# Performance work log

Hardware: AMD Instinct MI355X
Metric: run time of the kernel (lower is better)

The kernel has to match this reference:

```python
import jax, jax.numpy as jnp
import numpy as np

A = 40001         # atoms (+1 zero-padding row 0)
NB = 6            # max neighbors per atom (a2b width)
BN = 160001       # bonds (+1 zero-padding row 0)
ATOM_FDIM = 133
BOND_FDIM = 147
H = 300           # hidden_size (dim_embedding)
N_MOLS = 1000
A_SIZE = 40       # uniform atoms per molecule (a_scope)


def setup_inputs() -> dict:
    key = jax.random.key(0)
    ks = jax.random.split(key, 24)

    def w(k, shape, fan):
        return jax.random.normal(k, shape, dtype=jnp.float32) / np.sqrt(fan).astype(np.float32)

    f_atoms = jax.random.normal(ks[0], (A, ATOM_FDIM), dtype=jnp.float32).at[0].set(0.0)
    f_bonds = jax.random.normal(ks[1], (BN, BOND_FDIM), dtype=jnp.float32).at[0].set(0.0)
    a2b = jax.random.randint(ks[2], (A, NB), 0, BN, dtype=jnp.int32)
    b2a = jax.random.randint(ks[3], (BN,), 1, A, dtype=jnp.int32)
    b2revb = jax.random.randint(ks[4], (BN,), 1, BN, dtype=jnp.int32)

    return dict(
        f_atoms=f_atoms, f_bonds=f_bonds,
        Wi_atom=w(ks[5], (ATOM_FDIM, H), ATOM_FDIM),
        Wi_bond=w(ks[6], (BOND_FDIM, H), BOND_FDIM),
        Wh0=w(ks[7], (H, H), H),
        Wh1=w(ks[8], (H, H), H),
        W_lr=w(ks[9], (3 * H, H), 3 * H),
        W_o=w(ks[10], (2 * H, H), 2 * H),
        b_o=w(ks[11], (H,), H),
        gru_bias=w(ks[12], (H,), H),
        gWih_f=w(ks[13], (3 * H, H), H), gWhh_f=w(ks[14], (3 * H, H), H),
        gbih_f=w(ks[15], (3 * H,), H), gbhh_f=w(ks[16], (3 * H,), H),
        gWih_b=w(ks[17], (3 * H, H), H), gWhh_b=w(ks[18], (3 * H, H), H),
        gbih_b=w(ks[19], (3 * H,), H), gbhh_b=w(ks[20], (3 * H,), H),
        a2b=a2b, b2a=b2a, b2revb=b2revb,
        n_mols=N_MOLS, a_size=A_SIZE,
    )


def _gru_dir(x, h0, Wih, Whh, bih, bhh):
    """One direction of a torch-style GRU. x: [B,T,H], h0: [B,H] -> [B,T,H]."""
    xp = jnp.einsum('bth,gh->btg', x, Wih) + bih  # [B,T,3H], input proj precomputed

    def step(h, xt):
        gh = h @ Whh.T + bhh
        i_r, i_z, i_n = jnp.split(xt, 3, axis=-1)
        h_r, h_z, h_n = jnp.split(gh, 3, axis=-1)
        r = jax.nn.sigmoid(i_r + h_r)
        z = jax.nn.sigmoid(i_z + h_z)
        n = jnp.tanh(i_n + r * h_n)
        hn = (1.0 - z) * n + z * h
        return hn, hn

    _, ys = jax.lax.scan(step, h0, jnp.swapaxes(xp, 0, 1))
    return jnp.swapaxes(ys, 0, 1)


def _forward(f_atoms, f_bonds, Wi_atom, Wi_bond, Wh0, Wh1, W_lr, W_o, b_o, gru_bias,
             gWih_f, gWhh_f, gbih_f, gbhh_f, gWih_b, gWhh_b, gbih_b, gbhh_b,
             a2b, b2a, b2revb, n_mols, a_size):
    relu = jax.nn.relu
    input_atom = relu(f_atoms @ Wi_atom)              # [A,H]
    message_atom = input_atom
    input_bond = relu(f_bonds @ Wi_bond)              # [BN,H]
    message_bond = input_bond

    # depth-1 = 2 message passing steps (depth=3)
    for Wh in (Wh0, Wh1):
        nei = message_bond[a2b]                        # [A,NB,H] gather (index_select_ND)
        agg = nei.sum(axis=1) * nei.max(axis=1)        # sum * max neighbor aggregation
        message_atom = message_atom + agg
        mb = message_atom[b2a] - message_bond[b2revb]  # subtract reverse message
        message_bond = relu(input_bond + mb @ Wh)      # dropout p=0 -> identity

    nei = message_bond[a2b]
    agg = nei.sum(axis=1) * nei.max(axis=1)
    agg = jnp.concatenate([agg, message_atom, input_atom], axis=1) @ W_lr  # [A,H]

    # --- BatchGRU (uniform a_scope: mol i -> atoms [1+i*a_size, 1+(i+1)*a_size)) ---
    message = relu(agg + gru_bias)
    seqs = message[1:].reshape(n_mols, a_size, -1)     # padded per-mol sequences
    h0 = agg[1:].reshape(n_mols, a_size, -1).max(axis=1)  # init hidden = per-mol max
    out_f = _gru_dir(seqs, h0, gWih_f, gWhh_f, gbih_f, gbhh_f)
    out_b = _gru_dir(seqs[:, ::-1], h0, gWih_b, gWhh_b, gbih_b, gbhh_b)[:, ::-1]
    out = jnp.concatenate([out_f, out_b], axis=-1).reshape(n_mols * a_size, -1)  # [A-1,2H]
    pad0 = jnp.concatenate([message[0:1], message[0:1]], axis=1)  # padding row duplicated
    message2 = jnp.concatenate([pad0, out], axis=0)    # [A,2H]

    atom_hiddens = relu(message2 @ W_o + b_o)          # [A,H]
    mol_vecs = atom_hiddens[1:].reshape(n_mols, a_size, -1).mean(axis=1)  # [n_mols,H]
    return mol_vecs


def reference(f_atoms, f_bonds, Wi_atom, Wi_bond, Wh0, Wh1, W_lr, W_o, b_o, gru_bias,
              gWih_f, gWhh_f, gbih_f, gbhh_f, gWih_b, gWhh_b, gbih_b, gbhh_b,
              a2b, b2a, b2revb, n_mols, a_size):
    return _forward(f_atoms, f_bonds, Wi_atom, Wi_bond, Wh0, Wh1, W_lr, W_o, b_o, gru_bias,
                    gWih_f, gWhh_f, gbih_f, gbhh_f, gWih_b, gWhh_b, gbih_b, gbhh_b,
                    a2b, b2a, b2revb, n_mols, a_size)
```

## Files before the change

### kernel.cpp

```cpp
#include <hip/hip_runtime.h>
#include <math.h>

constexpr int A_TOT  = 40001;
constexpr int NB     = 6;
constexpr int BN_TOT = 160001;
constexpr int AF     = 133;
constexpr int BF     = 147;
constexpr int H      = 300;
constexpr int NMOL   = 1000;
constexpr int ASZ    = 40;

constexpr int PK_WH0 = 0;
constexpr int PK_WH1 = 90000;
constexpr int PK_WIB = 180000;
constexpr int PK_WIA = 224400;

template<int NR, int P>
__device__ __forceinline__ void gemv4(const float (*rows)[P], const float* __restrict__ W,
                                      int K, int f, float* __restrict__ acc)
{
    int k4 = 0;
    for (; k4 + 4 <= K; k4 += 4) {
        float w0 = W[(k4 + 0) * H + f];
        float w1 = W[(k4 + 1) * H + f];
        float w2 = W[(k4 + 2) * H + f];
        float w3 = W[(k4 + 3) * H + f];
#pragma unroll
        for (int i = 0; i < NR; ++i) {
            float4 b = *(const float4*)&rows[i][k4];
            acc[i] = fmaf(b.x, w0, fmaf(b.y, w1, fmaf(b.z, w2, fmaf(b.w, w3, acc[i]))));
        }
    }
    for (; k4 < K; ++k4) {
        float wv = W[k4 * H + f];
#pragma unroll
        for (int i = 0; i < NR; ++i) acc[i] = fmaf(rows[i][k4], wv, acc[i]);
    }
}

template<int NR, int P>
__device__ __forceinline__ void gemv4p(const float (*rows)[P], const float4* __restrict__ Pw,
                                       int K4, int f, float* __restrict__ acc)
{
#pragma clang loop unroll(disable)
    for (int k4i = 0; k4i < K4; ++k4i) {
        float4 w = Pw[k4i * 300 + f];
#pragma unroll
        for (int i = 0; i < NR; ++i) {
            float4 b = *(const float4*)&rows[i][k4i * 4];
            acc[i] = fmaf(b.x, w.x, fmaf(b.y, w.y, fmaf(b.z, w.z, fmaf(b.w, w.w, acc[i]))));
        }
    }
}

__global__ __launch_bounds__(256) void k_packmp(
    const float* __restrict__ s0, const float* __restrict__ s1,
    const float* __restrict__ s2, const float* __restrict__ s3,
    float* __restrict__ dout)
{
    const float* S[4] = {s0, s1, s2, s3};
    const int Ks[4]  = {300, 300, 147, 133};
    const int K4s[4] = {75, 75, 37, 34};
    const int off[4] = {PK_WH0, PK_WH1, PK_WIB, PK_WIA};
    int z = blockIdx.y;
    int o = blockIdx.x * 256 + threadIdx.x;
    int n = K4s[z] * 1200;
    if (o < n) {
        int k4 = o / 1200; int rem = o - k4 * 1200;
        int f = rem >> 2;  int j = rem & 3;
        int k = k4 * 4 + j;
        dout[off[z] + o] = (k < Ks[z]) ? S[z][(size_t)k * 300 + f] : 0.f;
    }
}

#define GA 4
__global__ __launch_bounds__(320) void k_msga1(
    const float* __restrict__ f_atoms, const float* __restrict__ f_bonds,
    const float4* __restrict__ PWia, const float4* __restrict__ PWib,
    const int* __restrict__ a2b, float* __restrict__ msgA1)
{
    __shared__ __align__(16) float fb[GA * NB][152];
    __shared__ __align__(16) float fa[GA][136];
    __shared__ int bidx[GA * NB];

    const int a0 = blockIdx.x * GA;
    const int tid = threadIdx.x;
    const int f = tid;

    if (tid < GA * NB) {
        int a = a0 + tid / NB;
        bidx[tid] = (a < A_TOT) ? a2b[a * NB + (tid % NB)] : 0;
    }
    __syncthreads();
    for (int idx = tid; idx < GA * NB * 148; idx += 320) {
        int i = idx / 148, k = idx - i * 148;
        fb[i][k] = (k < BF) ? f_bonds[(size_t)bidx[i] * BF + k] : 0.f;
    }
    for (int idx = tid; idx < GA * 136; idx += 320) {
        int l = idx / 136, k = idx - l * 136;
        int a = a0 + l;
        fa[l][k] = (a < A_TOT && k < AF) ? f_atoms[(size_t)a * AF + k] : 0.f;
    }
    __syncthreads();

    if (f < H) {
        float part[GA];
#pragma unroll
        for (int l = 0; l < GA; ++l) {
            float acc[NB];
#pragma unroll
            for (int j = 0; j < NB; ++j) acc[j] = 0.f;
            gemv4p<NB, 152>((const float (*)[152])&fb[l * NB], PWib, 37, f, acc);
            float s = 0.f, mx = -INFINITY;
#pragma unroll
            for (int j = 0; j < NB; ++j) {
                float x = fmaxf(acc[j], 0.f);
                s += x; mx = fmaxf(mx, x);
            }
            part[l] = s * mx;
        }
        float acc2[GA];
#pragma unroll
        for (int l = 0; l < GA; ++l) acc2[l] = 0.f;
        gemv4p<GA, 136>(fa, PWia, 34, f, acc2);
#pragma unroll
        for (int l = 0; l < GA; ++l) {
            int a = a0 + l;
            if (a < A_TOT) msgA1[(size_t)a * H + f] = fmaxf(acc2[l], 0.f) + part[l];
        }
    }
}

#define NR2 8
__global__ __launch_bounds__(320) void k_m1f(
    const float* __restrict__ f_bonds, const float4* __restrict__ PWib,
    const float4* __restrict__ PWh0, const float* __restrict__ msgA1,
    const int* __restrict__ b2a, const int* __restrict__ b2revb,
    float* __restrict__ m1)
{
    __shared__ __align__(16) float v[NR2][304];
    __shared__ __align__(16) float fbl[NR2][152];
    __shared__ int r_[NR2], q_[NR2], p_[NR2];

    const int r0 = blockIdx.x * NR2;
    const int tid = threadIdx.x;
    const int f = tid;

    if (tid < NR2) {
        int r = r0 + tid;
        if (r >= BN_TOT) r = 0;
        r_[tid] = r;
        q_[tid] = b2revb[r];
        p_[tid] = b2a[r];
    }
    __syncthreads();
    for (int idx = tid; idx < NR2 * 75; idx += 320) {
        int i = idx / 75, k4 = idx - i * 75;
        ((float4*)v[i])[k4] = ((const float4*)(msgA1 + (size_t)p_[i] * H))[k4];
    }
    for (int idx = tid; idx < NR2 * 148; idx += 320) {
        int i = idx / 148, k = idx - i * 148;
        fbl[i][k] = (k < BF) ? f_bonds[(size_t)q_[i] * BF + k] : 0.f;
    }
    __syncthreads();
    if (f < H) {
        float acc[NR2];
#pragma unroll
        for (int i = 0; i < NR2; ++i) acc[i] = 0.f;
        gemv4p<NR2, 152>(fbl, PWib, 37, f, acc);
#pragma unroll
        for (int i = 0; i < NR2; ++i) v[i][f] -= fmaxf(acc[i], 0.f);
    }
    __syncthreads();
    for (int idx = tid; idx < NR2 * 148; idx += 320) {
        int i = idx / 148, k = idx - i * 148;
        fbl[i][k] = (k < BF) ? f_bonds[(size_t)r_[i] * BF + k] : 0.f;
    }
    float accm[NR2];
#pragma unroll
    for (int i = 0; i < NR2; ++i) accm[i] = 0.f;
    if (f < H) gemv4p<NR2, 304>(v, PWh0, 75, f, accm);
    __syncthreads();
    if (f < H) {
        float accr[NR2];
#pragma unroll
        for (int i = 0; i < NR2; ++i) accr[i] = 0.f;
        gemv4p<NR2, 152>(fbl, PWib, 37, f, accr);
#pragma unroll
        for (int i = 0; i < NR2; ++i) {
            int r = r0 + i;
            if (r < BN_TOT)
                m1[(size_t)r * H + f] = fmaxf(fmaxf(accr[i], 0.f) + accm[i], 0.f);
        }
    }
}

__global__ __launch_bounds__(256) void k_msga2ef(
    const float* __restrict__ m1, const int* __restrict__ a2b, float* msgA)
{
    int idx = blockIdx.x * 256 + threadIdx.x;
    if (idx >= A_TOT * H) return;
    int a = idx / H;
    int f = idx - a * H;
    float s = 0.f, mx = -INFINITY;
#pragma unroll
    for (int j = 0; j < NB; ++j) {
        int r = a2b[a * NB + j];
        float v = m1[(size_t)r * H + f];
        s += v;
        mx = fmaxf(mx, v);
    }
    msgA[idx] += s * mx;
}

#define GC 2
#define RC (GC * NB)
__global__ __launch_bounds__(320) void k_aggl2f(
    const float* __restrict__ f_atoms, const float* __restrict__ f_bonds,
    const float4* __restrict__ PWia, const float4* __restrict__ PWib,
    const float4* __restrict__ PWh1, const float* __restrict__ W_lr,
    const float* __restrict__ msgA2, const float* __restrict__ m1,
    const int* __restrict__ a2b, const int* __restrict__ b2a,
    const int* __restrict__ b2revb, float* __restrict__ aggL)
{
    __shared__ __align__(16) float w[RC][304];
    __shared__ __align__(16) float fbl[RC][152];
    __shared__ __align__(16) float agg3r[GC][304];
    __shared__ __align__(16) float mA2r[GC][304];
    __shared__ __align__(16) float inAr[GC][304];
    __shared__ __align__(16) float fa[GC][136];
    __shared__ int b_[RC], rp_[RC], p2_[RC];

    const int a0 = blockIdx.x * GC;
    const int tid = threadIdx.x;
    const int f = tid;

    if (tid < RC) {
        int a = a0 + tid / NB;
        int b = (a < A_TOT) ? a2b[a * NB + (tid % NB)] : 0;
        b_[tid] = b;
        rp_[tid] = b2revb[b];
        p2_[tid] = b2a[b];
    }
    __syncthreads();
    for (int idx = tid; idx < RC * 75; idx += 320) {
        int i = idx / 75, k4 = idx - i * 75;
        float4 a4 = ((const float4*)(msgA2 + (size_t)p2_[i] * H))[k4];
        float4 b4 = ((const float4*)(m1 + (size_t)rp_[i] * H))[k4];
        ((float4*)w[i])[k4] = make_float4(a4.x - b4.x, a4.y - b4.y, a4.z - b4.z, a4.w - b4.w);
    }
    for (int idx = tid; idx < RC * 148; idx += 320) {
        int i = idx / 148, k = idx - i * 148;
        fbl[i][k] = (k < BF) ? f_bonds[(size_t)b_[i] * BF + k] : 0.f;
    }
    for (int idx = tid; idx < GC * 75; idx += 320) {
        int l = idx / 75, k4 = idx - l * 75;
        int a = a0 + l;
        ((float4*)mA2r[l])[k4] = (a < A_TOT) ? ((const float4*)(msgA2 + (size_t)a * H))[k4]
                                             : make_float4(0.f, 0.f, 0.f, 0.f);
    }
    for (int idx = tid; idx < GC * 136; idx += 320) {
        int l = idx / 136, k = idx - l * 136;
        int a = a0 + l;
        fa[l][k] = (a < A_TOT && k < AF) ? f_atoms[(size_t)a * AF + k] : 0.f;
    }
    __syncthreads();

    if (f < H) {
        float accm[RC];
#pragma unroll
        for (int i = 0; i < RC; ++i) accm[i] = 0.f;
        gemv4p<RC, 304>(w, PWh1, 75, f, accm);
        float accb[RC];
#pragma unroll
        for (int i = 0; i < RC; ++i) accb[i] = 0.f;
        gemv4p<RC, 152>(fbl, PWib, 37, f, accb);
#pragma unroll
        for (int l = 0; l < GC; ++l) {
            float s = 0.f, mx = -INFINITY;
#pragma unroll
            for (int j = 0; j < NB; ++j) {
                int i = l * NB + j;
                float m2 = fmaxf(fmaxf(accb[i], 0.f) + accm[i], 0.f);
                s += m2; mx = fmaxf(mx, m2);
            }
            agg3r[l][f] = s * mx;
        }
        float acc2[GC];
#pragma unroll
        for (int l = 0; l < GC; ++l) acc2[l] = 0.f;
        gemv4p<GC, 136>(fa, PWia, 34, f, acc2);
#pragma unroll
        for (int l = 0; l < GC; ++l) inAr[l][f] = fmaxf(acc2[l], 0.f);
    }
    __syncthreads();

    if (f < H) {
        float accL[GC];
#pragma unroll
        for (int l = 0; l < GC; ++l) accL[l] = 0.f;
        gemv4<GC, 304>(agg3r, W_lr,            H, f, accL);
        gemv4<GC, 304>(mA2r, W_lr + 300 * 300, H, f, accL);
        gemv4<GC, 304>(inAr, W_lr + 600 * 300, H, f, accL);
#pragma unroll
        for (int l = 0; l < GC; ++l) {
            int a = a0 + l;
            if (a < A_TOT) aggL[(size_t)a * H + f] = accL[l];
        }
    }
}

#define GB 4
#define RB (GB * NB)
__global__ __launch_bounds__(320) void k_msga2b(
    const float* __restrict__ f_bonds, const float* __restrict__ Wi_bond,
    const float* __restrict__ Wh0,
    const float* __restrict__ msgA1, float* __restrict__ msgA2,
    const int* __restrict__ a2b, const int* __restrict__ b2a,
    const int* __restrict__ b2revb)
{
    __shared__ __align__(16) float v[RB][304];
    __shared__ __align__(16) float fbl[RB][152];
    __shared__ int r_[RB], q_[RB], p_[RB];

    const int a0 = blockIdx.x * GB;
    const int tid = threadIdx.x;
    const int f = tid;

    if (tid < RB) {
        int a = a0 + tid / NB;
        int r = (a < A_TOT) ? a2b[a * NB + (tid % NB)] : 0;
        r_[tid] = r;
        q_[tid] = b2revb[r];
        p_[tid] = b2a[r];
    }
    __syncthreads();
    for (int idx = tid; idx < RB * 75; idx += 320) {
        int i = idx / 75, k4 = idx - i * 75;
        ((float4*)v[i])[k4] = ((const float4*)(msgA1 + (size_t)p_[i] * H))[k4];
    }
    for (int idx = tid; idx < RB * BF; idx += 320) {
        int i = idx / BF, k = idx - i * BF;
        fbl[i][k] = f_bonds[(size_t)q_[i] * BF + k];
    }
    __syncthreads();
    if (f < H) {
        float acc[RB];
#pragma unroll
        for (int i = 0; i < RB; ++i) acc[i] = 0.f;
        gemv4<RB, 152>(fbl, Wi_bond, BF, f, acc);
#pragma unroll
        for (int i = 0; i < RB; ++i) v[i][f] -= fmaxf(acc[i], 0.f);
    }
    __syncthreads();
    for (int idx = tid; idx < RB * BF; idx += 320) {
        int i = idx / BF, k = idx - i * BF;
        fbl[i][k] = f_bonds[(size_t)r_[i] * BF + k];
    }
    float accm[RB];
#pragma unroll
    for (int i = 0; i < RB; ++i) accm[i] = 0.f;
    if (f < H) gemv4<RB, 304>(v, Wh0, H, f, accm);
    __syncthreads();
    if (f < H) {
        float accr[RB];
#pragma unroll
        for (int i = 0; i < RB; ++i) accr[i] = 0.f;
        gemv4<RB, 152>(fbl, Wi_bond, BF, f, accr);
#pragma unroll
        for (int l = 0; l < GB; ++l) {
            float s = 0.f, mx = -INFINITY;
#pragma unroll
            for (int j = 0; j < NB; ++j) {
                int i = l * NB + j;
                float m1 = fmaxf(fmaxf(accr[i], 0.f) + accm[i], 0.f);
                s += m1; mx = fmaxf(mx, m1);
            }
            int a = a0 + l;
            if (a < A_TOT)
                msgA2[(size_t)a * H + f] = msgA1[(size_t)a * H + f] + s * mx;
        }
    }
}

#define GCB 2
#define RCB (GCB * NB)
__global__ __launch_bounds__(320) void k_agglb(
    const float* __restrict__ f_atoms, const float* __restrict__ f_bonds,
    const float* __restrict__ Wi_atom, const float* __restrict__ Wi_bond,
    const float* __restrict__ Wh0, const float* __restrict__ Wh1,
    const float* __restrict__ W_lr,
    const float* __restrict__ msgA1, const float* __restrict__ msgA2,
    const int* __restrict__ a2b, const int* __restrict__ b2a,
    const int* __restrict__ b2revb, float* __restrict__ aggL)
{
    __shared__ __align__(16) float u[RCB][304];
    __shared__ __align__(16) float w[RCB][304];
    __shared__ __align__(16) float fbl[RCB][152];
    __shared__ __align__(16) float agg3r[GCB][304];
    __shared__ __align__(16) float mA2r[GCB][304];
    __shared__ __align__(16) float inAr[GCB][304];
    __shared__ __align__(16) float fa[GCB][136];
    __shared__ int b_[RCB], rp_[RCB], p1_[RCB], q1_[RCB], p2_[RCB];

    const int a0 = blockIdx.x * GCB;
    const int tid = threadIdx.x;
    const int f = tid;

    if (tid < RCB) {
        int a = a0 + tid / NB;
        int b = (a < A_TOT) ? a2b[a * NB + (tid % NB)] : 0;
        int rp = b2revb[b];
        b_[tid] = b; rp_[tid] = rp;
        p1_[tid] = b2a[rp]; q1_[tid] = b2revb[rp]; p2_[tid] = b2a[b];
    }
    __syncthreads();
    for (int idx = tid; idx < RCB * 75; idx += 320) {
        int i = idx / 75, k4 = idx - i * 75;
        ((float4*)u[i])[k4] = ((const float4*)(msgA1 + (size_t)p1_[i] * H))[k4];
        ((float4*)w[i])[k4] = ((const float4*)(msgA2 + (size_t)p2_[i] * H))[k4];
    }
    for (int idx = tid; idx < RCB * BF; idx += 320) {
        int i = idx / BF, k = idx - i * BF;
        fbl[i][k] = f_bonds[(size_t)q1_[i] * BF + k];
    }
    for (int idx = tid; idx < GCB * 75; idx += 320) {
        int l = idx / 75, k4 = idx - l * 75;
        int a = a0 + l;
        ((float4*)mA2r[l])[k4] = (a < A_TOT) ? ((const float4*)(msgA2 + (size_t)a * H))[k4]
                                             : make_float4(0.f, 0.f, 0.f, 0.f);
    }
    for (int idx = tid; idx < GCB * AF; idx += 320) {
        int l = idx / AF, k = idx - l * AF;
        int a = a0 + l;
        fa[l][k] = (a < A_TOT) ? f_atoms[(size_t)a * AF + k] : 0.f;
    }
    __syncthreads();
    if (f < H) {
        float acc[RCB];
#pragma unroll
        for (int i = 0; i < RCB; ++i) acc[i] = 0.f;
        gemv4<RCB, 152>(fbl, Wi_bond, BF, f, acc);
#pragma unroll
        for (int i = 0; i < RCB; ++i) u[i][f] -= fmaxf(acc[i], 0.f);
    }
    __syncthreads();
    for (int idx = tid; idx < RCB * BF; idx += 320) {
        int i = idx / BF, k = idx - i * BF;
        fbl[i][k] = f_bonds[(size_t)rp_[i] * BF + k];
    }
    __syncthreads();
    if (f < H) {
        float accm[RCB], accr[RCB];
#pragma unroll
        for (int i = 0; i < RCB; ++i) { accm[i] = 0.f; accr[i] = 0.f; }
        gemv4<RCB, 304>(u, Wh0, H, f, accm);
        gemv4<RCB, 152>(fbl, Wi_bond, BF, f, accr);
#pragma unroll
        for (int i = 0; i < RCB; ++i)
            w[i][f] -= fmaxf(fmaxf(accr[i], 0.f) + accm[i], 0.f);
    }
    __syncthreads();
    for (int idx = tid; idx < RCB * BF; idx += 320) {
        int i = idx / BF, k = idx - i * BF;
        fbl[i][k] = f_bonds[(size_t)b_[i] * BF + k];
    }
    __syncthreads();
    if (f < H) {
        float accm[RCB], accb[RCB];
#pragma unroll
        for (int i = 0; i < RCB; ++i) { accm[i] = 0.f; accb[i] = 0.f; }
        gemv4<RCB, 304>(w, Wh1, H, f, accm);
        gemv4<RCB, 152>(fbl, Wi_bond, BF, f, accb);
#pragma unroll
        for (int l = 0; l < GCB; ++l) {
            float s = 0.f, mx = -INFINITY;
#pragma unroll
            for (int j = 0; j < NB; ++j) {
                int i = l * NB + j;
                float m2 = fmaxf(fmaxf(accb[i], 0.f) + accm[i], 0.f);
                s += m2; mx = fmaxf(mx, m2);
            }
            agg3r[l][f] = s * mx;
        }
        float acc2[GCB];
#pragma unroll
        for (int l = 0; l < GCB; ++l) acc2[l] = 0.f;
        gemv4<GCB, 136>(fa, Wi_atom, AF, f, acc2);
#pragma unroll
        for (int l = 0; l < GCB; ++l) inAr[l][f] = fmaxf(acc2[l], 0.f);
    }
    __syncthreads();
    if (f < H) {
        float accL[GCB];
#pragma unroll
        for (int l = 0; l < GCB; ++l) accL[l] = 0.f;
        gemv4<GCB, 304>(agg3r, W_lr,            H, f, accL);
        gemv4<GCB, 304>(mA2r, W_lr + 300 * 300, H, f, accL);
        gemv4<GCB, 304>(inAr, W_lr + 600 * 300, H, f, accL);
#pragma unroll
        for (int l = 0; l < GCB; ++l) {
            int a = a0 + l;
            if (a < A_TOT) aggL[(size_t)a * H + f] = accL[l];
        }
    }
}

__global__ __launch_bounds__(256) void k_pack4(
    const float* __restrict__ s0, const float* __restrict__ s1,
    const float* __restrict__ s2, const float* __restrict__ s3,
    float* __restrict__ d0, float* __restrict__ d1,
    float* __restrict__ d2, float* __restrict__ d3)
{
    const float* S[4] = {s0, s1, s2, s3};
    float* D[4] = {d0, d1, d2, d3};
    int z = blockIdx.y;
    int o = blockIdx.x * 256 + threadIdx.x;
    if (o < 270000) {
        int k4 = o / 3600; int rem = o - k4 * 3600;
        int g = rem / 1200; int rem2 = rem - g * 1200;
        int fx = rem2 >> 2; int kk = rem2 & 3;
        int k = k4 * 4 + kk;
        D[z][o] = S[z][(size_t)(g * 300 + fx) * 300 + k];
    }
}

__global__ __launch_bounds__(256) void prep_kernel(
    float* aggL, const float* __restrict__ gru_bias, float* __restrict__ h0)
{
    int m = blockIdx.x;
    for (int f = threadIdx.x; f < H; f += 256) {
        float b = gru_bias[f];
        float mx = -INFINITY;
        for (int t = 0; t < ASZ; ++t) {
            size_t o = (size_t)(1 + m * ASZ + t) * H + f;
            float v = aggL[o];
            mx = fmaxf(mx, v);
            aggL[o] = fmaxf(v + b, 0.f);
        }
        h0[(size_t)m * H + f] = mx;
    }
}

__device__ __forceinline__ float dev_sigmoid(float x) {
    return 1.f / (1.f + __expf(-x));
}
__device__ __forceinline__ float dev_tanh(float x) {
    return 1.f - 2.f / (__expf(2.f * x) + 1.f);
}

#define GM 8
__global__ __launch_bounds__(320) void k_gru_all(
    const float* __restrict__ msg,
    const float* __restrict__ Pih_f, const float* __restrict__ Phh_f,
    const float* __restrict__ bih_f, const float* __restrict__ bhh_f,
    const float* __restrict__ Pih_b, const float* __restrict__ Phh_b,
    const float* __restrict__ bih_b, const float* __restrict__ bhh_b,
    const float* __restrict__ h0, float* __restrict__ out_f,
    float* __restrict__ out_b)
{
    __shared__ __align__(16) float hs[GM][304];
    __shared__ __align__(16) float ms[2][GM][304];

    const int bid  = blockIdx.x;
    const int xcd  = bid & 7;
    const int slot = bid >> 3;
    const int dir  = xcd >> 2;
    const int lg   = (xcd & 3) * 32 + slot;
    const int m0   = lg * GM;
    if (m0 >= NMOL) return;

    const float* Pih = dir ? Pih_b : Pih_f;
    const float* Phh = dir ? Phh_b : Phh_f;
    const float* bih = dir ? bih_b : bih_f;
    const float* bhh = dir ? bhh_b : bhh_f;
    float* out       = dir ? out_b : out_f;

    const int tid  = threadIdx.x;
    const bool act = tid < H;
    const int f    = act ? tid : (H - 1);

    for (int idx = tid; idx < GM * 75; idx += 320) {
        int i = idx / 75, k4 = idx - i * 75;
        int m = m0 + i;
        ((float4*)hs[i])[k4] = (m < NMOL) ? ((const float4*)(h0 + (size_t)m * H))[k4]
                                          : make_float4(0.f, 0.f, 0.f, 0.f);
    }
    {
        const int t0 = dir ? (ASZ - 1) : 0;
        for (int idx = tid; idx < GM * 75; idx += 320) {
            int i = idx / 75, k4 = idx - i * 75;
            int m = m0 + i;
            ((float4*)ms[0][i])[k4] = (m < NMOL)
                ? ((const float4*)(msg + (size_t)(m * ASZ + t0) * H))[k4]
                : make_float4(0.f, 0.f, 0.f, 0.f);
        }
    }

    float bR = 0.f, bZ = 0.f, bIN = 0.f, bHN = 0.f;
    if (act) {
        bR  = bih[f] + bhh[f];
        bZ  = bih[300 + f] + bhh[300 + f];
        bIN = bih[600 + f];
        bHN = bhh[600 + f];
    }
    const float* pi = Pih + (size_t)f * 4;
    const float* ph = Phh + (size_t)f * 4;

    for (int s = 0; s < ASZ; ++s) {
        const int cur = s & 1;
        const int t = dir ? (ASZ - 1 - s) : s;
        __syncthreads();

        float4 st0 = make_float4(0.f, 0.f, 0.f, 0.f);
        float4 st1 = make_float4(0.f, 0.f, 0.f, 0.f);
        const bool more = (s + 1 < ASZ);
        if (more) {
            const int tn = dir ? (ASZ - 2 - s) : (s + 1);
            {
                int i = tid / 75, k4 = tid - i * 75;
                int m = m0 + i;
                if (m < NMOL)
                    st0 = ((const float4*)(msg + (size_t)(m * ASZ + tn) * H))[k4];
            }
            {
                int idx = tid + 320;
                if (idx < GM * 75) {
                    int i = idx / 75, k4 = idx - i * 75;
                    int m = m0 + i;
                    if (m < NMOL)
                        st1 = ((const float4*)(msg + (size_t)(m * ASZ + tn) * H))[k4];
                }
            }
        }

        float aR[GM], aZ[GM], aIN[GM], aHN[GM];
#pragma unroll
        for (int i = 0; i < GM; ++i) { aR[i] = 0.f; aZ[i] = 0.f; aIN[i] = 0.f; aHN[i] = 0.f; }

        float4 wiR = *(const float4*)(pi);
        float4 wiZ = *(const float4*)(pi + 1200);
        float4 wiN = *(const float4*)(pi + 2400);
        float4 whR = *(const float4*)(ph);
        float4 whZ = *(const float4*)(ph + 1200);
        float4 whN = *(const float4*)(ph + 2400);

        for (int k4i = 0; k4i < 75; ++k4i) {
            const int kn = k4i + (k4i < 74 ? 1 : 0);
            const float* pin = pi + (size_t)kn * 3600;
            const float* phn = ph + (size_t)kn * 3600;
            float4 nR = *(const float4*)(pin);
            float4 nZ = *(const float4*)(pin + 1200);
            float4 nN = *(const float4*)(pin + 2400);
            float4 oR = *(const float4*)(phn);
            float4 oZ = *(const float4*)(phn + 1200);
            float4 oN = *(const float4*)(phn + 2400);

            const int k4 = k4i * 4;
#pragma unroll
            for (int i = 0; i < GM; ++i) {
                float4 m4 = *(const float4*)&ms[cur][i][k4];
                float4 h4 = *(const float4*)&hs[i][k4];
                aR[i]  = fmaf(m4.x, wiR.x, fmaf(m4.y, wiR.y, fmaf(m4.z, wiR.z, fmaf(m4.w, wiR.w, aR[i]))));
                aR[i]  = fmaf(h4.x, whR.x, fmaf(h4.y, whR.y, fmaf(h4.z, whR.z, fmaf(h4.w, whR.w, aR[i]))));
                aZ[i]  = fmaf(m4.x, wiZ.x, fmaf(m4.y, wiZ.y, fmaf(m4.z, wiZ.z, fmaf(m4.w, wiZ.w, aZ[i]))));
                aZ[i]  = fmaf(h4.x, whZ.x, fmaf(h4.y, whZ.y, fmaf(h4.z, whZ.z, fmaf(h4.w, whZ.w, aZ[i]))));
                aIN[i] = fmaf(m4.x, wiN.x, fmaf(m4.y, wiN.y, fmaf(m4.z, wiN.z, fmaf(m4.w, wiN.w, aIN[i]))));
                aHN[i] = fmaf(h4.x, whN.x, fmaf(h4.y, whN.y, fmaf(h4.z, whN.z, fmaf(h4.w, whN.w, aHN[i]))));
            }
            wiR = nR; wiZ = nZ; wiN = nN;
            whR = oR; whZ = oZ; whN = oN;
        }
        __syncthreads();

        if (act) {
#pragma unroll
            for (int i = 0; i < GM; ++i) {
                int m = m0 + i;
                if (m < NMOL) {
                    float r = dev_sigmoid(aR[i] + bR);
                    float z = dev_sigmoid(aZ[i] + bZ);
                    float n = dev_tanh(aIN[i] + bIN + r * (aHN[i] + bHN));
                    float hn = (1.f - z) * n + z * hs[i][f];
                    hs[i][f] = hn;
                    __builtin_nontemporal_store(hn, out + (size_t)(m * ASZ + t) * H + f);
                }
            }
        }
        if (more) {
            const int nxt = cur ^ 1;
            {
                int i = tid / 75, k4 = tid - i * 75;
                ((float4*)ms[nxt][i])[k4] = st0;
            }
            {
                int idx = tid + 320;
                if (idx < GM * 75) {
                    int i = idx / 75, k4 = idx - i * 75;
                    ((float4*)ms[nxt][i])[k4] = st1;
                }
            }
        }
    }
}

__global__ __launch_bounds__(256) void gemm_wo(
    const float* __restrict__ A0, const float* __restrict__ A1,
    const float* __restrict__ W, float* __restrict__ C,
    const float* __restrict__ bias)
{
    const int M = NMOL * ASZ, K2 = 600, N = H;
    __shared__ float As[16][64];
    __shared__ float Bs[16][64];
    const int tx = threadIdx.x, ty = threadIdx.y;
    const int tid = ty * 16 + tx;
    const int m0 = blockIdx.x * 64, n0 = blockIdx.y * 64;
    const int am = tid >> 2, ak = (tid & 3) * 4;
    const int bk = tid >> 4, bn = (tid & 15) * 4;
    const int arow = m0 + am;

    float acc[4][4];
#pragma unroll
    for (int i = 0; i < 4; ++i)
#pragma unroll
        for (int j = 0; j < 4; ++j) acc[i][j] = 0.f;

    for (int k0 = 0; k0 < K2; k0 += 16) {
#pragma unroll
        for (int j = 0; j < 4; ++j) {
            int k = k0 + ak + j;
            float v = 0.f;
            if (arow < M && k < K2)
                v = (k < 300) ? A0[(size_t)arow * 300 + k]
                              : A1[(size_t)arow * 300 + (k - 300)];
            As[ak + j][am] = v;
        }
#pragma unroll
        for (int j = 0; j < 4; ++j) {
            int k = k0 + bk, n = n0 + bn + j;
            Bs[bk][bn + j] = (k < K2 && n < N) ? W[(size_t)k * N + n] : 0.f;
        }
        __syncthreads();
#pragma unroll
        for (int kk = 0; kk < 16; ++kk) {
            float4 av = *(const float4*)&As[kk][ty * 4];
            float4 bv = *(const float4*)&Bs[kk][tx * 4];
            float a4[4] = {av.x, av.y, av.z, av.w};
            float b4[4] = {bv.x, bv.y, bv.z, bv.w};
#pragma unroll
            for (int i = 0; i < 4; ++i)
#pragma unroll
                for (int j = 0; j < 4; ++j)
                    acc[i][j] = fmaf(a4[i], b4[j], acc[i][j]);
        }
        __syncthreads();
    }
#pragma unroll
    for (int i = 0; i < 4; ++i) {
        int m = m0 + ty * 4 + i;
        if (m >= M) continue;
#pragma unroll
        for (int j = 0; j < 4; ++j) {
            int n = n0 + tx * 4 + j;
            if (n >= N) continue;
            C[(size_t)m * N + n] = fmaxf(acc[i][j] + bias[n], 0.f);
        }
    }
}

__global__ __launch_bounds__(256) void mean_kernel(
    const float* __restrict__ hid, float* __restrict__ out)
{
    int m = blockIdx.x;
    for (int f = threadIdx.x; f < H; f += 256) {
        float s = 0.f;
        for (int t = 0; t < ASZ; ++t)
            s += hid[(size_t)(m * ASZ + t) * H + f];
        out[(size_t)m * H + f] = s * (1.f / 40.f);
    }
}

extern "C" void kernel_launch(void* const* d_in, const int* in_sizes, int n_in,
                              void* d_out, int out_size, void* d_ws, size_t ws_size,
                              hipStream_t stream)
{
    const float* f_atoms  = (const float*)d_in[0];
    const float* f_bonds  = (const float*)d_in[1];
    const float* Wi_atom  = (const float*)d_in[2];
    const float* Wi_bond  = (const float*)d_in[3];
    const float* Wh0      = (const float*)d_in[4];
    const float* Wh1      = (const float*)d_in[5];
    const float* W_lr     = (const float*)d_in[6];
    const float* W_o      = (const float*)d_in[7];
    const float* b_o      = (const float*)d_in[8];
    const float* gru_bias = (const float*)d_in[9];
    const float* gWih_f   = (const float*)d_in[10];
    const float* gWhh_f   = (const float*)d_in[11];
    const float* gbih_f   = (const float*)d_in[12];
    const float* gbhh_f   = (const float*)d_in[13];
    const float* gWih_b   = (const float*)d_in[14];
    const float* gWhh_b   = (const float*)d_in[15];
    const float* gbih_b   = (const float*)d_in[16];
    const float* gbhh_b   = (const float*)d_in[17];
    const int*   a2b      = (const int*)d_in[18];
    const int*   b2a      = (const int*)d_in[19];
    const int*   b2revb   = (const int*)d_in[20];

    char* wsb = (char*)d_ws;
    const bool bigws = (ws_size >= (size_t)288003600);

    float* dscratch = (float*)d_out;
    {
        dim3 g((90000 + 255) / 256, 4);
        k_packmp<<<g, 256, 0, stream>>>(Wh0, Wh1, Wi_bond, Wi_atom, dscratch);
    }
    const float4* PWh0 = (const float4*)(dscratch + PK_WH0);
    const float4* PWh1 = (const float4*)(dscratch + PK_WH1);
    const float4* PWib = (const float4*)(dscratch + PK_WIB);
    const float4* PWia = (const float4*)(dscratch + PK_WIA);

    float *aggLp, *outfp, *outbp, *h0p, *P0, *P1, *P2, *P3, *hidp;

    if (bigws) {
        float* msgA = (float*)wsb;
        float* aggL = (float*)(wsb + 48001200);
        float* m1   = (float*)(wsb + 96002400);
        outfp = (float*)(wsb + 96002400);
        outbp = (float*)(wsb + 144002400);
        P0 = (float*)(wsb + 192002400);
        P1 = P0 + 270000; P2 = P1 + 270000; P3 = P2 + 270000;
        h0p = (float*)(wsb + 196322400);
        aggLp = aggL; hidp = msgA;

        k_msga1<<<(A_TOT + GA - 1) / GA, 320, 0, stream>>>(
            f_atoms, f_bonds, PWia, PWib, a2b, msgA);
        k_m1f<<<(BN_TOT + NR2 - 1) / NR2, 320, 0, stream>>>(
            f_bonds, PWib, PWh0, msgA, b2a, b2revb, m1);
        k_msga2ef<<<(A_TOT * H + 255) / 256, 256, 0, stream>>>(m1, a2b, msgA);
        k_aggl2f<<<(A_TOT + GC - 1) / GC, 320, 0, stream>>>(
            f_atoms, f_bonds, PWia, PWib, PWh1, W_lr,
            msgA, m1, a2b, b2a, b2revb, aggL);
    } else {
        float* ws = (float*)d_ws;
        float* msgA1 = ws;
        float* msgA2 = ws + 12000300;
        float* aggL  = ws + 24000600;
        outfp = ws + 36000900;
        outbp = ws + 48000900;
        h0p   = ws;
        P0 = ws + 300000; P1 = ws + 570000; P2 = ws + 840000; P3 = ws + 1110000;
        aggLp = aggL; hidp = msgA2;

        k_msga1<<<(A_TOT + GA - 1) / GA, 320, 0, stream>>>(
            f_atoms, f_bonds, PWia, PWib, a2b, msgA1);
        k_msga2b<<<(A_TOT + GB - 1) / GB, 320, 0, stream>>>(
            f_bonds, Wi_bond, Wh0, msgA1, msgA2, a2b, b2a, b2revb);
        k_agglb<<<(A_TOT + GCB - 1) / GCB, 320, 0, stream>>>(
            f_atoms, f_bonds, Wi_atom, Wi_bond, Wh0, Wh1, W_lr,
            msgA1, msgA2, a2b, b2a, b2revb, aggL);
    }

    {
        dim3 g((270000 + 255) / 256, 4);
        k_pack4<<<g, 256, 0, stream>>>(gWih_f, gWhh_f, gWih_b, gWhh_b,
                                       P0, P1, P2, P3);
    }

    prep_kernel<<<NMOL, 256, 0, stream>>>(aggLp, gru_bias, h0p);

    k_gru_all<<<256, 320, 0, stream>>>(
        aggLp + H, P0, P1, gbih_f, gbhh_f, P2, P3, gbih_b, gbhh_b,
        h0p, outfp, outbp);

    {
        dim3 grid((NMOL * ASZ + 63) / 64, (H + 63) / 64);
        dim3 block(16, 16);
        gemm_wo<<<grid, block, 0, stream>>>(outfp, outbp, W_o, hidp, b_o);
    }

    mean_kernel<<<NMOL, 256, 0, stream>>>(hidp, (float*)d_out);
}
```

Before: 7.322 ms.

## Distribute Wh1 over the gathered difference by projecting atoms and bonds beforehand

Uses linearity of (msgA2[src] - m1[rev]) @ Wh1: a new row-tiled GEMM kernel projects all atom messages and all bond messages through Wh1 once, and the aggregation kernel then gathers and subtracts the already projected rows. This replaces a per-gathered-bond GEMV (six bonds per atom) with one projection per atom plus one per bond, using 16-row tiles for better weight reuse. The bond projection is written in place over m1, and the aggregation output is written over msgA. The trade-off is two extra kernel launches and extra full passes over the atom and bond buffers.

```diff
diff --git a/kernel.cpp b/kernel.cpp
--- a/kernel.cpp
+++ b/kernel.cpp
@@ -73,6 +73,36 @@
     }
 }
 
+#define RG 16
+__global__ __launch_bounds__(320) void k_gemm_rp(
+    const float* __restrict__ src, float* __restrict__ dst,
+    const float4* __restrict__ Pw, int M)
+{
+    __shared__ __align__(16) float rows[RG][304];
+    const int r0 = blockIdx.x * RG;
+    const int tid = threadIdx.x;
+    const int f = tid;
+
+    for (int idx = tid; idx < RG * 75; idx += 320) {
+        int i = idx / 75, k4 = idx - i * 75;
+        int r = r0 + i;
+        ((float4*)rows[i])[k4] = (r < M) ? ((const float4*)(src + (size_t)r * H))[k4]
+                                         : make_float4(0.f, 0.f, 0.f, 0.f);
+    }
+    __syncthreads();
+    if (f < H) {
+        float acc[RG];
+#pragma unroll
+        for (int i = 0; i < RG; ++i) acc[i] = 0.f;
+        gemv4p<RG, 304>(rows, Pw, 75, f, acc);
+#pragma unroll
+        for (int i = 0; i < RG; ++i) {
+            int r = r0 + i;
+            if (r < M) dst[(size_t)r * H + f] = acc[i];
+        }
+    }
+}
+
 #define GA 4
 __global__ __launch_bounds__(320) void k_msga1(
     const float* __restrict__ f_atoms, const float* __restrict__ f_bonds,
@@ -215,13 +245,13 @@
 
 #define GC 2
 #define RC (GC * NB)
-__global__ __launch_bounds__(320) void k_aggl2f(
+__global__ __launch_bounds__(320) void k_aggl3f(
     const float* __restrict__ f_atoms, const float* __restrict__ f_bonds,
     const float4* __restrict__ PWia, const float4* __restrict__ PWib,
-    const float4* __restrict__ PWh1, const float* __restrict__ W_lr,
-    const float* __restrict__ msgA2, const float* __restrict__ m1,
+    const float* __restrict__ A2W, const float* __restrict__ M1W,
+    const float* __restrict__ W_lr, const float* __restrict__ msgA2,
     const int* __restrict__ a2b, const int* __restrict__ b2a,
-    const int* __restrict__ b2revb, float* __restrict__ aggL)
+    const int* __restrict__ b2revb, float* __restrict__ aggLout)
 {
     __shared__ __align__(16) float w[RC][304];
     __shared__ __align__(16) float fbl[RC][152];
@@ -245,8 +275,8 @@
     __syncthreads();
     for (int idx = tid; idx < RC * 75; idx += 320) {
         int i = idx / 75, k4 = idx - i * 75;
-        float4 a4 = ((const float4*)(msgA2 + (size_t)p2_[i] * H))[k4];
-        float4 b4 = ((const float4*)(m1 + (size_t)rp_[i] * H))[k4];
+        float4 a4 = ((const float4*)(A2W + (size_t)p2_[i] * H))[k4];
+        float4 b4 = ((const float4*)(M1W + (size_t)rp_[i] * H))[k4];
         ((float4*)w[i])[k4] = make_float4(a4.x - b4.x, a4.y - b4.y, a4.z - b4.z, a4.w - b4.w);
     }
     for (int idx = tid; idx < RC * 148; idx += 320) {
@@ -267,10 +297,6 @@
     __syncthreads();
 
     if (f < H) {
-        float accm[RC];
-#pragma unroll
-        for (int i = 0; i < RC; ++i) accm[i] = 0.f;
-        gemv4p<RC, 304>(w, PWh1, 75, f, accm);
         float accb[RC];
 #pragma unroll
         for (int i = 0; i < RC; ++i) accb[i] = 0.f;
@@ -281,7 +307,7 @@
 #pragma unroll
             for (int j = 0; j < NB; ++j) {
                 int i = l * NB + j;
-                float m2 = fmaxf(fmaxf(accb[i], 0.f) + accm[i], 0.f);
+                float m2 = fmaxf(fmaxf(accb[i], 0.f) + w[i][f], 0.f);
                 s += m2; mx = fmaxf(mx, m2);
             }
             agg3r[l][f] = s * mx;
@@ -305,7 +331,7 @@
 #pragma unroll
         for (int l = 0; l < GC; ++l) {
             int a = a0 + l;
-            if (a < A_TOT) aggL[(size_t)a * H + f] = accL[l];
+            if (a < A_TOT) aggLout[(size_t)a * H + f] = accL[l];
         }
     }
 }
@@ -823,23 +849,27 @@
 
     if (bigws) {
         float* msgA = (float*)wsb;
-        float* aggL = (float*)(wsb + 48001200);
+        float* A2W  = (float*)(wsb + 48001200);
         float* m1   = (float*)(wsb + 96002400);
         outfp = (float*)(wsb + 96002400);
         outbp = (float*)(wsb + 144002400);
         P0 = (float*)(wsb + 192002400);
         P1 = P0 + 270000; P2 = P1 + 270000; P3 = P2 + 270000;
         h0p = (float*)(wsb + 196322400);
-        aggLp = aggL; hidp = msgA;
+        aggLp = msgA; hidp = A2W;
 
         k_msga1<<<(A_TOT + GA - 1) / GA, 320, 0, stream>>>(
             f_atoms, f_bonds, PWia, PWib, a2b, msgA);
         k_m1f<<<(BN_TOT + NR2 - 1) / NR2, 320, 0, stream>>>(
             f_bonds, PWib, PWh0, msgA, b2a, b2revb, m1);
         k_msga2ef<<<(A_TOT * H + 255) / 256, 256, 0, stream>>>(m1, a2b, msgA);
-        k_aggl2f<<<(A_TOT + GC - 1) / GC, 320, 0, stream>>>(
-            f_atoms, f_bonds, PWia, PWib, PWh1, W_lr,
-            msgA, m1, a2b, b2a, b2revb, aggL);
+
+        k_gemm_rp<<<(A_TOT + RG - 1) / RG, 320, 0, stream>>>(msgA, A2W, PWh1, A_TOT);
+        k_gemm_rp<<<(BN_TOT + RG - 1) / RG, 320, 0, stream>>>(m1, m1, PWh1, BN_TOT);
+
+        k_aggl3f<<<(A_TOT + GC - 1) / GC, 320, 0, stream>>>(
+            f_atoms, f_bonds, PWia, PWib, A2W, m1 , W_lr,
+            msgA, a2b, b2a, b2revb, msgA);
     } else {
         float* ws = (float*)d_ws;
         float* msgA1 = ws;
```

Result: faster. 7.048 ms (-3.7%).
